# Kernel optimization log

Measured on AMD Instinct MI355X. Metric: run time of the kernel, lower is better.

The kernel has to match this reference:

```python
import jax, jax.numpy as jnp
import numpy as np

N = 10000      # num nodes
R = 16         # num relations
NB = 30        # num bases (hardcoded in source: num_bases=30)
E = 160000     # num edges
IN, HID, OUT = 256, 256, 128


def rgcn_conv(x, src, dst, etype, basis, comp, root, bias):
    """PyG RGCNConv with basis decomposition, aggr='mean' (per relation), root weight + bias."""
    # relation weights from basis decomposition: W_r = sum_b comp[r,b] * basis[b]
    W = jnp.einsum('rb,bio->rio', comp, basis)            # [R, in, out]
    xw = jnp.einsum('ni,rio->rno', x, W)                  # [R, N, out]
    msg = xw[etype, src]                                  # [E, out] gather per edge
    # per-(dst, relation) mean aggregation, then sum over relations
    seg = dst * R + etype                                 # combined segment key
    cnt = jax.ops.segment_sum(jnp.ones((msg.shape[0],), msg.dtype), seg, num_segments=N * R)
    msg = msg / jnp.maximum(cnt[seg], 1.0)[:, None]       # zero-degree -> 0 (matches scatter-mean)
    agg = jax.ops.segment_sum(msg, dst, num_segments=N)   # [N, out]
    return agg + x @ root + bias


def setup_inputs() -> dict:
    key = jax.random.key(0)
    ks = jax.random.split(key, 11)
    g = lambda k, shape, s: jax.random.normal(k, shape, jnp.float32) * s
    s1 = (2.0 / (IN + HID)) ** 0.5
    s2 = (2.0 / (HID + OUT)) ** 0.5
    return dict(
        x=g(ks[0], (N, IN), 1.0),
        edge_index=jax.random.randint(ks[1], (2, E), 0, N),
        edge_type=jax.random.randint(ks[2], (E,), 0, R),
        basis1=g(ks[3], (NB, IN, HID), s1),
        comp1=g(ks[4], (R, NB), 1.0 / NB ** 0.5),
        root1=g(ks[5], (IN, HID), s1),
        bias1=jnp.zeros((HID,), jnp.float32),
        basis2=g(ks[6], (NB, HID, OUT), s2),
        comp2=g(ks[7], (R, NB), 1.0 / NB ** 0.5),
        root2=g(ks[8], (HID, OUT), s2),
        bias2=jnp.zeros((OUT,), jnp.float32),
    )


def reference(x, edge_index, edge_type, basis1, comp1, root1, bias1,
              basis2, comp2, root2, bias2):
    src, dst = edge_index[0], edge_index[1]
    h = jax.nn.relu(rgcn_conv(x, src, dst, edge_type, basis1, comp1, root1, bias1))
    return rgcn_conv(h, src, dst, edge_type, basis2, comp2, root2, bias2)
```

## Files before the change

### kernel.cpp

```cpp
#include <hip/hip_runtime.h>
#include <hip/hip_bf16.h>

#define NN 10000
#define MP 10112
#define RR 16
#define NBASE 30
#define EE 160000
#define HIDF 256
#define OUTF 128
#define NSEG (NN * RR)

typedef __attribute__((ext_vector_type(8))) short bf16x8;
typedef __attribute__((ext_vector_type(4))) short s16x4;
typedef __attribute__((ext_vector_type(4))) float f32x4;

static __device__ __forceinline__ short f2bf(float f) {
    union { float f; unsigned u; } v; v.f = f;
    unsigned r = v.u + 0x7FFFu + ((v.u >> 16) & 1u);
    return (short)(r >> 16);
}
static __device__ __forceinline__ float bf2f(short s) {
    union { unsigned u; float f; } v;
    v.u = ((unsigned)(unsigned short)s) << 16;
    return v.f;
}
static __device__ __forceinline__ void gl16(const short* g, short* l) {
    __builtin_amdgcn_global_load_lds((const __attribute__((address_space(1))) void*)g,
                                     (__attribute__((address_space(3))) void*)l, 16, 0, 0);
}

template <int OUT>
__global__ void wtr_k(const float* __restrict__ basis, const float* __restrict__ comp,
                      const float* __restrict__ root, short* __restrict__ WT) {
    __shared__ short t[32][34];
    const int i0 = blockIdx.x * 32, n0 = blockIdx.y * 32;
    const int r = n0 / OUT, o0 = n0 % OUT;
    const int tx = threadIdx.x & 31, ty = threadIdx.x >> 5;
    #pragma unroll
    for (int dy = 0; dy < 32; dy += 8) {
        const int i = i0 + ty + dy, o = o0 + tx;
        float v;
        if (r < RR) {
            float s = 0.f;
            #pragma unroll
            for (int b = 0; b < NBASE; b++)
                s += comp[r * NBASE + b] * basis[((long)b * 256 + i) * OUT + o];
            v = s;
        } else {
            v = root[(long)i * OUT + o];
        }
        t[ty + dy][tx] = f2bf(v);
    }
    __syncthreads();
    #pragma unroll
    for (int dy = 0; dy < 32; dy += 8)
        WT[(long)(n0 + ty + dy) * 256 + i0 + tx] = t[tx][ty + dy];
}

__global__ void count_k(const int* __restrict__ dst, const int* __restrict__ et,
                        int* __restrict__ cnt) {
    int e = blockIdx.x * 256 + threadIdx.x;
    if (e < EE) atomicAdd(&cnt[dst[e] * RR + et[e]], 1);
}

__global__ void inv_k(const int* __restrict__ cnt, float* __restrict__ invc) {
    int i = blockIdx.x * 256 + threadIdx.x;
    if (i < NSEG) invc[i] = 1.f / (float)max(cnt[i], 1);
}

__global__ void scan1_k(const int* __restrict__ cnt, int* __restrict__ incl,
                        int* __restrict__ bsum) {
    __shared__ int s[256];
    int i = blockIdx.x * 256 + threadIdx.x;
    int v = (i < NSEG) ? cnt[i] : 0;
    s[threadIdx.x] = v;
    __syncthreads();
    for (int off = 1; off < 256; off <<= 1) {
        int u = (threadIdx.x >= off) ? s[threadIdx.x - off] : 0;
        __syncthreads();
        s[threadIdx.x] += u;
        __syncthreads();
    }
    if (i < NSEG) incl[i] = s[threadIdx.x];
    if (threadIdx.x == 255) bsum[blockIdx.x] = s[255];
}

__global__ void scan2_k(int* __restrict__ bsum, int nb) {
    __shared__ int s[1024];
    int t = threadIdx.x;
    s[t] = (t < nb) ? bsum[t] : 0;
    __syncthreads();
    for (int off = 1; off < 1024; off <<= 1) {
        int u = (t >= off) ? s[t - off] : 0;
        __syncthreads();
        s[t] += u;
        __syncthreads();
    }
    if (t < nb) bsum[t] = s[t];
}

__global__ void scan3_k(const int* __restrict__ cnt, const int* __restrict__ incl,
                        const int* __restrict__ bsum, int* __restrict__ row_ptr,
                        int* __restrict__ fillpos) {
    int i = blockIdx.x * 256 + threadIdx.x;
    if (i >= NSEG) return;
    int off = (blockIdx.x > 0) ? bsum[blockIdx.x - 1] : 0;
    int ex = off + incl[i] - cnt[i];
    row_ptr[i] = ex;
    fillpos[i] = ex;
    if (i == 0) row_ptr[NSEG] = EE;
}

__global__ void fill_k(const int* __restrict__ src, const int* __restrict__ dst,
                       const int* __restrict__ et, int* __restrict__ fillpos,
                       const float* __restrict__ invc,
                       int* __restrict__ eoff1, int* __restrict__ eoff2,
                       float* __restrict__ wgt) {
    int e = blockIdx.x * 256 + threadIdx.x;
    if (e < EE) {
        int s = src[e], t = et[e];
        int seg = dst[e] * RR + t;
        int p = atomicAdd(&fillpos[seg], 1);
        eoff1[p] = s * (17 * HIDF) + t * HIDF;
        eoff2[p] = s * (17 * OUTF) + t * OUTF;
        wgt[p] = invc[seg];
    }
}

__global__ void cvtbf_k(const float* __restrict__ X, short* __restrict__ Y) {
    int i = blockIdx.x * 256 + threadIdx.x;
    if (i >= NN * 64) return;
    float4 v = *(const float4*)(X + (long)i * 4);
    s16x4 pk = { f2bf(v.x), f2bf(v.y), f2bf(v.z), f2bf(v.w) };
    *(s16x4*)&Y[(long)i * 4] = pk;
}

template <int NTOT>
__global__ __launch_bounds__(256, 4) void gemm_xw_k(const short* __restrict__ A,
                                                    const short* __restrict__ WT,
                                                    short* __restrict__ XW) {
    constexpr int NBN = NTOT / 128;
    __shared__ __align__(16) short smem[128 * 132];
    short* As = smem;
    short* Bs = smem + 8192;

    const int nwg = gridDim.x;
    const int q = nwg >> 3, r = nwg & 7;
    const int orig = blockIdx.x;
    const int xcd = orig & 7, wi = orig >> 3;
    const int wgid = (xcd < r ? xcd * (q + 1) : r * (q + 1) + (xcd - r) * q) + wi;
    const int m0 = (wgid / NBN) * 128;
    const int n0 = (wgid % NBN) * 128;

    const int tid = threadIdx.x;
    const int lane = tid & 63;
    const int w = tid >> 6;
    const int wr = w >> 1, wc = w & 1;
    const int al = lane & 15;
    const int cl = lane >> 4;

    int gsrc[4];
    #pragma unroll
    for (int i = 0; i < 4; i++) {
        int ci = i * 256 + tid;
        int row = ci >> 3;
        gsrc[i] = row * 256 + (((ci & 7) ^ (row & 7)) << 3);
    }

    int aoff[4][2], boff[4][2];
    #pragma unroll
    for (int f = 0; f < 4; f++)
        #pragma unroll
        for (int k2 = 0; k2 < 2; k2++) {
            int ra = wr * 64 + f * 16 + al;
            aoff[f][k2] = (ra << 6) + ((((k2 << 2) | cl) ^ (ra & 7)) << 3);
            int rb = wc * 64 + f * 16 + al;
            boff[f][k2] = (rb << 6) + ((((k2 << 2) | cl) ^ (rb & 7)) << 3);
        }

    f32x4 acc[4][4] = {};
    const short* abase = A + (long)m0 * 256;
    const short* bbase = WT + (long)n0 * 256;

    #pragma unroll
    for (int kk = 0; kk < 256; kk += 64) {
        #pragma unroll
        for (int i = 0; i < 4; i++)
            gl16(abase + kk + gsrc[i], &As[i * 2048 + w * 512]);
        #pragma unroll
        for (int i = 0; i < 4; i++)
            gl16(bbase + kk + gsrc[i], &Bs[i * 2048 + w * 512]);
        __syncthreads();

        bf16x8 a[4][2], b[4][2];
        #pragma unroll
        for (int f = 0; f < 4; f++)
            #pragma unroll
            for (int k2 = 0; k2 < 2; k2++) {
                a[f][k2] = *(const bf16x8*)&As[aoff[f][k2]];
                b[f][k2] = *(const bf16x8*)&Bs[boff[f][k2]];
            }
        #pragma unroll
        for (int k2 = 0; k2 < 2; k2++)
            #pragma unroll
            for (int fm = 0; fm < 4; fm++)
                #pragma unroll
                for (int fn = 0; fn < 4; fn++)
                    acc[fm][fn] = __builtin_amdgcn_mfma_f32_16x16x32_bf16(
                        a[fm][k2], b[fn][k2], acc[fm][fn], 0, 0, 0);
        __syncthreads();
    }

    #pragma unroll
    for (int fm = 0; fm < 4; fm++) {
        const int rowb = wr * 64 + fm * 16 + (cl << 2);
        #pragma unroll
        for (int fn = 0; fn < 4; fn++) {
            const int col = wc * 64 + fn * 16 + al;
            #pragma unroll
            for (int j = 0; j < 4; j++)
                smem[(rowb + j) * 132 + col] = f2bf(acc[fm][fn][j]);
        }
    }
    __syncthreads();

    #pragma unroll
    for (int pass = 0; pass < 8; pass++) {
        int c = pass * 256 + tid;
        int row = c >> 4, qq = c & 15;
        uint4 v = *(const uint4*)&smem[row * 132 + qq * 8];
        *(uint4*)&XW[(long)(m0 + row) * NTOT + n0 + qq * 8] = v;
    }
}

template <int OUT, bool L1>
__global__ void aggh_k(const int* __restrict__ rowp, const int* __restrict__ eoff,
                       const float* __restrict__ wgt, const short* __restrict__ XW,
                       const float* __restrict__ bias, short* __restrict__ Hout,
                       float* __restrict__ Fout) {
    constexpr int NTOT = 17 * OUT;
    const int n = (blockIdx.x * 256 + threadIdx.x) >> 6;
    const int lane = threadIdx.x & 63;
    if (n >= NN) return;
    const int b = rowp[n * 16], e = rowp[n * 16 + 16];

    if (L1) {
        float a0 = 0.f, a1 = 0.f, a2 = 0.f, a3 = 0.f;
        int j = b;
        for (; j + 1 < e; j += 2) {
            int o0 = eoff[j], o1 = eoff[j + 1];
            float w0 = wgt[j], w1 = wgt[j + 1];
            s16x4 v0 = *(const s16x4*)&XW[(long)o0 + lane * 4];
            s16x4 v1 = *(const s16x4*)&XW[(long)o1 + lane * 4];
            a0 += w0 * bf2f(v0.x) + w1 * bf2f(v1.x);
            a1 += w0 * bf2f(v0.y) + w1 * bf2f(v1.y);
            a2 += w0 * bf2f(v0.z) + w1 * bf2f(v1.z);
            a3 += w0 * bf2f(v0.w) + w1 * bf2f(v1.w);
        }
        if (j < e) {
            int o0 = eoff[j]; float w0 = wgt[j];
            s16x4 v0 = *(const s16x4*)&XW[(long)o0 + lane * 4];
            a0 += w0 * bf2f(v0.x); a1 += w0 * bf2f(v0.y);
            a2 += w0 * bf2f(v0.z); a3 += w0 * bf2f(v0.w);
        }
        s16x4 rt = *(const s16x4*)&XW[(long)n * NTOT + 16 * OUT + lane * 4];
        f32x4 bb = *(const f32x4*)&bias[lane * 4];
        a0 = fmaxf(a0 + bf2f(rt.x) + bb.x, 0.f);
        a1 = fmaxf(a1 + bf2f(rt.y) + bb.y, 0.f);
        a2 = fmaxf(a2 + bf2f(rt.z) + bb.z, 0.f);
        a3 = fmaxf(a3 + bf2f(rt.w) + bb.w, 0.f);
        s16x4 pk = { f2bf(a0), f2bf(a1), f2bf(a2), f2bf(a3) };
        *(s16x4*)&Hout[(long)n * OUT + lane * 4] = pk;
    } else {
        float a0 = 0.f, a1 = 0.f;
        int j = b;
        for (; j + 1 < e; j += 2) {
            int o0 = eoff[j], o1 = eoff[j + 1];
            float w0 = wgt[j], w1 = wgt[j + 1];
            unsigned v0 = *(const unsigned*)&XW[(long)o0 + lane * 2];
            unsigned v1 = *(const unsigned*)&XW[(long)o1 + lane * 2];
            a0 += w0 * bf2f((short)(v0 & 0xffff)) + w1 * bf2f((short)(v1 & 0xffff));
            a1 += w0 * bf2f((short)(v0 >> 16)) + w1 * bf2f((short)(v1 >> 16));
        }
        if (j < e) {
            int o0 = eoff[j]; float w0 = wgt[j];
            unsigned v0 = *(const unsigned*)&XW[(long)o0 + lane * 2];
            a0 += w0 * bf2f((short)(v0 & 0xffff));
            a1 += w0 * bf2f((short)(v0 >> 16));
        }
        unsigned rt = *(const unsigned*)&XW[(long)n * NTOT + 16 * OUT + lane * 2];
        a0 += bf2f((short)(rt & 0xffff)) + bias[lane * 2];
        a1 += bf2f((short)(rt >> 16)) + bias[lane * 2 + 1];
        float2 st = { a0, a1 };
        *(float2*)&Fout[(long)n * OUT + lane * 2] = st;
    }
}

extern "C" void kernel_launch(void* const* d_in, const int* in_sizes, int n_in,
                              void* d_out, int out_size, void* d_ws, size_t ws_size,
                              hipStream_t stream) {
    const float* x      = (const float*)d_in[0];
    const int*   ei     = (const int*)d_in[1];
    const int*   et     = (const int*)d_in[2];
    const float* basis1 = (const float*)d_in[3];
    const float* comp1  = (const float*)d_in[4];
    const float* root1  = (const float*)d_in[5];
    const float* bias1  = (const float*)d_in[6];
    const float* basis2 = (const float*)d_in[7];
    const float* comp2  = (const float*)d_in[8];
    const float* root2  = (const float*)d_in[9];
    const float* bias2  = (const float*)d_in[10];
    const int* src = ei;
    const int* dst = ei + EE;

    char* p = (char*)d_ws;
    auto take = [&](size_t bytes) { char* q = p; p += (bytes + 255) & ~(size_t)255; return q; };
    short* XW    = (short*)take((size_t)MP * 17 * HIDF * 2);
    short* WT1   = (short*)take((size_t)17 * HIDF * 256 * 2);
    short* WT2   = (short*)take((size_t)17 * OUTF * 256 * 2);
    short* Xbf   = (short*)take((size_t)MP * 256 * 2);
    short* Hbf   = (short*)take((size_t)MP * 256 * 2);
    int*   cnt   = (int*)take((size_t)NSEG * 4);
    float* invc  = (float*)take((size_t)NSEG * 4);
    int*   incl  = (int*)take((size_t)NSEG * 4);
    int*   rowp  = (int*)take((size_t)(NSEG + 1) * 4);
    int*   fpos  = (int*)take((size_t)NSEG * 4);
    int*   bsum  = (int*)take(1024 * 4);
    int*   eoff1 = (int*)take((size_t)EE * 4);
    int*   eoff2 = (int*)take((size_t)EE * 4);
    float* wgt   = (float*)take((size_t)EE * 4);

    const int NB1 = (NSEG + 255) / 256;

    hipMemsetAsync(cnt, 0, (size_t)NSEG * 4, stream);

    {
        dim3 g1(256 / 32, 17 * HIDF / 32), g2(256 / 32, 17 * OUTF / 32);
        wtr_k<HIDF><<<g1, 256, 0, stream>>>(basis1, comp1, root1, WT1);
        wtr_k<OUTF><<<g2, 256, 0, stream>>>(basis2, comp2, root2, WT2);
    }

    count_k<<<(EE + 255) / 256, 256, 0, stream>>>(dst, et, cnt);
    inv_k<<<NB1, 256, 0, stream>>>(cnt, invc);
    scan1_k<<<NB1, 256, 0, stream>>>(cnt, incl, bsum);
    scan2_k<<<1, 1024, 0, stream>>>(bsum, NB1);
    scan3_k<<<NB1, 256, 0, stream>>>(cnt, incl, bsum, rowp, fpos);
    fill_k<<<(EE + 255) / 256, 256, 0, stream>>>(src, dst, et, fpos, invc, eoff1, eoff2, wgt);

    cvtbf_k<<<(NN * 64 + 255) / 256, 256, 0, stream>>>(x, Xbf);

    gemm_xw_k<17 * HIDF><<<(MP / 128) * (17 * HIDF / 128), 256, 0, stream>>>(Xbf, WT1, XW);
    aggh_k<HIDF, true><<<(NN * 64) / 256, 256, 0, stream>>>(rowp, eoff1, wgt, XW, bias1, Hbf, nullptr);

    gemm_xw_k<17 * OUTF><<<(MP / 128) * (17 * OUTF / 128), 256, 0, stream>>>(Hbf, WT2, XW);
    aggh_k<OUTF, false><<<(NN * 64) / 256, 256, 0, stream>>>(rowp, eoff2, wgt, XW, bias2, nullptr, (float*)d_out);
}
```

Baseline: 146.5 us.

## Double-buffer GEMM K-loop with 32-wide tiles and fold inverse-count into scan

```diff
diff --git a/kernel.cpp b/kernel.cpp
--- a/kernel.cpp
+++ b/kernel.cpp
@@ -63,11 +63,6 @@
     if (e < EE) atomicAdd(&cnt[dst[e] * RR + et[e]], 1);
 }
 
-__global__ void inv_k(const int* __restrict__ cnt, float* __restrict__ invc) {
-    int i = blockIdx.x * 256 + threadIdx.x;
-    if (i < NSEG) invc[i] = 1.f / (float)max(cnt[i], 1);
-}
-
 __global__ void scan1_k(const int* __restrict__ cnt, int* __restrict__ incl,
                         int* __restrict__ bsum) {
     __shared__ int s[256];
@@ -101,13 +96,15 @@
 
 __global__ void scan3_k(const int* __restrict__ cnt, const int* __restrict__ incl,
                         const int* __restrict__ bsum, int* __restrict__ row_ptr,
-                        int* __restrict__ fillpos) {
+                        int* __restrict__ fillpos, float* __restrict__ invc) {
     int i = blockIdx.x * 256 + threadIdx.x;
     if (i >= NSEG) return;
+    int c = cnt[i];
     int off = (blockIdx.x > 0) ? bsum[blockIdx.x - 1] : 0;
-    int ex = off + incl[i] - cnt[i];
+    int ex = off + incl[i] - c;
     row_ptr[i] = ex;
     fillpos[i] = ex;
+    invc[i] = 1.f / (float)max(c, 1);
     if (i == 0) row_ptr[NSEG] = EE;
 }
 
@@ -140,9 +137,7 @@
                                                     const short* __restrict__ WT,
                                                     short* __restrict__ XW) {
     constexpr int NBN = NTOT / 128;
-    __shared__ __align__(16) short smem[128 * 132];
-    short* As = smem;
-    short* Bs = smem + 8192;
+    __shared__ __align__(16) short smem[16384];
 
     const int nwg = gridDim.x;
     const int q = nwg >> 3, r = nwg & 7;
@@ -159,77 +154,87 @@
     const int al = lane & 15;
     const int cl = lane >> 4;
 
-    int gsrc[4];
-    #pragma unroll
-    for (int i = 0; i < 4; i++) {
+    int gsrc[2];
+    #pragma unroll
+    for (int i = 0; i < 2; i++) {
         int ci = i * 256 + tid;
-        int row = ci >> 3;
-        gsrc[i] = row * 256 + (((ci & 7) ^ (row & 7)) << 3);
-    }
-
-    int aoff[4][2], boff[4][2];
-    #pragma unroll
-    for (int f = 0; f < 4; f++)
-        #pragma unroll
-        for (int k2 = 0; k2 < 2; k2++) {
-            int ra = wr * 64 + f * 16 + al;
-            aoff[f][k2] = (ra << 6) + ((((k2 << 2) | cl) ^ (ra & 7)) << 3);
-            int rb = wc * 64 + f * 16 + al;
-            boff[f][k2] = (rb << 6) + ((((k2 << 2) | cl) ^ (rb & 7)) << 3);
-        }
+        int row = ci >> 2;
+        gsrc[i] = row * 256 + (((ci & 3) ^ ((row >> 1) & 3)) << 3);
+    }
+
+    int aoff[4], boff[4];
+    #pragma unroll
+    for (int f = 0; f < 4; f++) {
+        int ra = wr * 64 + f * 16 + al;
+        aoff[f] = (ra << 5) + (((cl ^ ((ra >> 1) & 3))) << 3);
+        int rb = wc * 64 + f * 16 + al;
+        boff[f] = (rb << 5) + (((cl ^ ((rb >> 1) & 3))) << 3);
+    }
 
     f32x4 acc[4][4] = {};
     const short* abase = A + (long)m0 * 256;
     const short* bbase = WT + (long)n0 * 256;
 
     #pragma unroll
-    for (int kk = 0; kk < 256; kk += 64) {
+    for (int i = 0; i < 2; i++) {
+        gl16(abase + gsrc[i], &smem[i * 2048 + w * 512]);
+        gl16(bbase + gsrc[i], &smem[4096 + i * 2048 + w * 512]);
+    }
+    __syncthreads();
+
+    constexpr int NT = 8;
+    #pragma unroll
+    for (int t = 0; t < NT; ++t) {
+        const int cur = t & 1;
+        if (t + 1 < NT) {
+            const int kk = (t + 1) * 32;
+            #pragma unroll
+            for (int i = 0; i < 2; i++) {
+                gl16(abase + kk + gsrc[i], &smem[(cur ^ 1) * 8192 + i * 2048 + w * 512]);
+                gl16(bbase + kk + gsrc[i], &smem[(cur ^ 1) * 8192 + 4096 + i * 2048 + w * 512]);
+            }
+        }
+        const short* As = &smem[cur * 8192];
+        const short* Bs = &smem[cur * 8192 + 4096];
+        bf16x8 a[4], b[4];
         #pragma unroll
-        for (int i = 0; i < 4; i++)
-            gl16(abase + kk + gsrc[i], &As[i * 2048 + w * 512]);
+        for (int f = 0; f < 4; f++) {
+            a[f] = *(const bf16x8*)&As[aoff[f]];
+            b[f] = *(const bf16x8*)&Bs[boff[f]];
+        }
         #pragma unroll
-        for (int i = 0; i < 4; i++)
-            gl16(bbase + kk + gsrc[i], &Bs[i * 2048 + w * 512]);
-        __syncthreads();
-
-        bf16x8 a[4][2], b[4][2];
+        for (int fm = 0; fm < 4; fm++)
+            #pragma unroll
+            for (int fn = 0; fn < 4; fn++)
+                acc[fm][fn] = __builtin_amdgcn_mfma_f32_16x16x32_bf16(
+                    a[fm], b[fn], acc[fm][fn], 0, 0, 0);
+        __syncthreads();
+    }
+
+    #pragma unroll
+    for (int h = 0; h < 2; h++) {
+        if (wr == h) {
+            #pragma unroll
+            for (int fm = 0; fm < 4; fm++) {
+                const int rowb = fm * 16 + (cl << 2);
+                #pragma unroll
+                for (int fn = 0; fn < 4; fn++) {
+                    const int col = wc * 64 + fn * 16 + al;
+                    #pragma unroll
+                    for (int j = 0; j < 4; j++)
+                        smem[(rowb + j) * 132 + col] = f2bf(acc[fm][fn][j]);
+                }
+            }
+        }
+        __syncthreads();
         #pragma unroll
-        for (int f = 0; f < 4; f++)
-            #pragma unroll
-            for (int k2 = 0; k2 < 2; k2++) {
-                a[f][k2] = *(const bf16x8*)&As[aoff[f][k2]];
-                b[f][k2] = *(const bf16x8*)&Bs[boff[f][k2]];
-            }
-        #pragma unroll
-        for (int k2 = 0; k2 < 2; k2++)
-            #pragma unroll
-            for (int fm = 0; fm < 4; fm++)
-                #pragma unroll
-                for (int fn = 0; fn < 4; fn++)
-                    acc[fm][fn] = __builtin_amdgcn_mfma_f32_16x16x32_bf16(
-                        a[fm][k2], b[fn][k2], acc[fm][fn], 0, 0, 0);
-        __syncthreads();
-    }
-
-    #pragma unroll
-    for (int fm = 0; fm < 4; fm++) {
-        const int rowb = wr * 64 + fm * 16 + (cl << 2);
-        #pragma unroll
-        for (int fn = 0; fn < 4; fn++) {
-            const int col = wc * 64 + fn * 16 + al;
-            #pragma unroll
-            for (int j = 0; j < 4; j++)
-                smem[(rowb + j) * 132 + col] = f2bf(acc[fm][fn][j]);
-        }
-    }
-    __syncthreads();
-
-    #pragma unroll
-    for (int pass = 0; pass < 8; pass++) {
-        int c = pass * 256 + tid;
-        int row = c >> 4, qq = c & 15;
-        uint4 v = *(const uint4*)&smem[row * 132 + qq * 8];
-        *(uint4*)&XW[(long)(m0 + row) * NTOT + n0 + qq * 8] = v;
+        for (int pass = 0; pass < 4; pass++) {
+            int c = pass * 256 + tid;
+            int row = c >> 4, qq = c & 15;
+            uint4 v = *(const uint4*)&smem[row * 132 + qq * 8];
+            *(uint4*)&XW[(long)(m0 + h * 64 + row) * NTOT + n0 + qq * 8] = v;
+        }
+        __syncthreads();
     }
 }
 
@@ -341,10 +346,9 @@
     }
 
     count_k<<<(EE + 255) / 256, 256, 0, stream>>>(dst, et, cnt);
-    inv_k<<<NB1, 256, 0, stream>>>(cnt, invc);
     scan1_k<<<NB1, 256, 0, stream>>>(cnt, incl, bsum);
     scan2_k<<<1, 1024, 0, stream>>>(bsum, NB1);
-    scan3_k<<<NB1, 256, 0, stream>>>(cnt, incl, bsum, rowp, fpos);
+    scan3_k<<<NB1, 256, 0, stream>>>(cnt, incl, bsum, rowp, fpos, invc);
     fill_k<<<(EE + 255) / 256, 256, 0, stream>>>(src, dst, et, fpos, invc, eoff1, eoff2, wgt);
 
     cvtbf_k<<<(NN * 64 + 255) / 256, 256, 0, stream>>>(x, Xbf);
```

Result: no change. 146.4 us (-0.1%).
